# Kernel optimization log

Hardware: AMD Instinct MI355X
Metric: run time of the kernel (lower is better)

## Reference

```python
import jax, jax.numpy as jnp
import numpy as np


def _global_softmax(h):
    # Faithful to soft(): exp over ALL elements, divide by total sum (flattened).
    m = jnp.max(h)  # global max for numerical stability
    e = jnp.exp(h - m)
    return e / jnp.sum(e)


def setup_inputs() -> dict:
    key = jax.random.key(0)
    ks = jax.random.split(key, 7)
    B = 262144
    return {
        "x": jax.random.normal(ks[0], (B, 256), dtype=jnp.float32),
        "wz1": jax.random.normal(ks[1], (256, 64), dtype=jnp.float32) * 0.05,
        "b1": jax.random.normal(ks[2], (1, 64), dtype=jnp.float32),
        "wz2": jax.random.normal(ks[3], (64, 16), dtype=jnp.float32) * 0.1,
        "b2": jax.random.normal(ks[4], (1, 16), dtype=jnp.float32),
        "wz3": jax.random.normal(ks[5], (16, 4), dtype=jnp.float32) * 0.2,
        "b3": jax.random.normal(ks[6], (1, 4), dtype=jnp.float32),
    }


def reference(x, wz1, b1, wz2, b2, wz3, b3):
    h = jax.nn.relu(x @ wz1 + b1)          # [B,64]
    h = jnp.tanh(h @ wz2 + b2)             # [B,16]
    h = h @ wz3 + b3                       # [B,4]
    return _global_softmax(h)              # normalized over all B*4 elements
```

## Files before the change

### kernel.cpp

```cpp
#include <hip/hip_runtime.h>


typedef _Float16 half8 __attribute__((ext_vector_type(8)));
typedef _Float16 half4 __attribute__((ext_vector_type(4)));
typedef float f32x4 __attribute__((ext_vector_type(4)));

#define GRID 256
#define TPB  512
#define TROWS 64

#define XS  264
#define WS  264
#define H1S 72
#define W2S 72

#define SCALE_IN 256.0f
#define SCALE_W  2048.0f
#define INV_SC   (1.0f/524288.0f)

#define OFF_XH  0
#define OFF_XL  (OFF_XH + TROWS*XS*2)
#define OFF_W1H (OFF_XL + TROWS*XS*2)
#define OFF_W1L (OFF_W1H + 64*WS*2)
#define OFF_H1H (OFF_W1L + 64*WS*2)
#define OFF_H1L (OFF_H1H + TROWS*H1S*2)
#define OFF_W2H (OFF_H1L + TROWS*H1S*2)
#define OFF_W2L (OFF_W2H + 16*W2S*2)
#define OFF_SUM (OFF_W2L + 16*W2S*2)
#define SMEM_BYTES (OFF_SUM + 64*4)

extern __shared__ char smem_raw[];

#define MFMA16(a,b,c) __builtin_amdgcn_mfma_f32_16x16x32_f16((a),(b),(c),0,0,0)

__device__ __forceinline__ void lds_barrier() {
    asm volatile("s_waitcnt lgkmcnt(0)\ns_barrier" ::: "memory");
}

__global__ __launch_bounds__(TPB, 2) void fused_mlp(
    const float* __restrict__ x,
    const float* __restrict__ wz1, const float* __restrict__ b1,
    const float* __restrict__ wz2, const float* __restrict__ b2,
    const float* __restrict__ wz3, const float* __restrict__ b3,
    float* __restrict__ Eout, float* __restrict__ block_sums,
    int ntiles)
{
    _Float16* xh  = (_Float16*)(smem_raw + OFF_XH);
    _Float16* xl  = (_Float16*)(smem_raw + OFF_XL);
    _Float16* w1h = (_Float16*)(smem_raw + OFF_W1H);
    _Float16* w1l = (_Float16*)(smem_raw + OFF_W1L);
    _Float16* h1h = (_Float16*)(smem_raw + OFF_H1H);
    _Float16* h1l = (_Float16*)(smem_raw + OFF_H1L);
    _Float16* w2h = (_Float16*)(smem_raw + OFF_W2H);
    _Float16* w2l = (_Float16*)(smem_raw + OFF_W2L);
    float* sums   = (float*)(smem_raw + OFF_SUM);

    const int tid  = threadIdx.x;
    const int lane = tid & 63;
    const int wid  = __builtin_amdgcn_readfirstlane(tid >> 6);
    const int l15  = lane & 15;
    const int g8   = (lane >> 4) * 8;

    const size_t blk_row0 = (size_t)blockIdx.x * ntiles * TROWS;

    float4 xv[8];
    {
        const float4* xg = (const float4*)(x + blk_row0 * 256);
        #pragma unroll
        for (int c = 0; c < 8; ++c) xv[c] = xg[c * TPB + tid];
    }

    {
        const float4* wg = (const float4*)wz1;
        #pragma unroll
        for (int c = 0; c < 8; ++c) {
            const int q = c * TPB + tid;
            const float4 v = wg[q];
            const int k = q >> 4, n0 = (q & 15) * 4;
            const float vv[4] = {v.x, v.y, v.z, v.w};
            #pragma unroll
            for (int i = 0; i < 4; ++i) {
                const float s = vv[i] * SCALE_W;
                const _Float16 h = (_Float16)s;
                w1h[(n0 + i) * WS + k] = h;
                w1l[(n0 + i) * WS + k] = (_Float16)(s - (float)h);
            }
        }
        if (tid < 256) {
            const float4 v = ((const float4*)wz2)[tid];
            const int k = tid >> 2, c0 = (tid & 3) * 4;
            const float vv[4] = {v.x, v.y, v.z, v.w};
            #pragma unroll
            for (int i = 0; i < 4; ++i) {
                const float s = vv[i] * SCALE_W;
                const _Float16 h = (_Float16)s;
                w2h[(c0 + i) * W2S + k] = h;
                w2l[(c0 + i) * W2S + k] = (_Float16)(s - (float)h);
            }
        }
    }

    const int rt  = wid >> 1;
    const int ntp = wid & 1;
    const int col0 = (2 * ntp) * 16 + l15;
    const int col1 = (2 * ntp + 1) * 16 + l15;
    const float b1v0 = b1[col0], b1v1 = b1[col1];
    float b2v[4], w3v[4][4];
    #pragma unroll
    for (int i = 0; i < 4; ++i) {
        const int c2 = (lane >> 4) * 4 + i;
        b2v[i] = b2[c2];
        #pragma unroll
        for (int c3 = 0; c3 < 4; ++c3) w3v[i][c3] = wz3[c2 * 4 + c3];
    }
    const float b3v[4] = {b3[0], b3[1], b3[2], b3[3]};

    lds_barrier();

    half8 Bh[8][2];
    #pragma unroll
    for (int kt = 0; kt < 8; ++kt) {
        Bh[kt][0] = *(const half8*)(w1h + col0 * WS + kt * 32 + g8);
        Bh[kt][1] = *(const half8*)(w1h + col1 * WS + kt * 32 + g8);
    }
    half8 A2h[2], A2l[2];
    #pragma unroll
    for (int kt = 0; kt < 2; ++kt) {
        A2h[kt] = *(const half8*)(w2h + l15 * W2S + kt * 32 + g8);
        A2l[kt] = *(const half8*)(w2l + l15 * W2S + kt * 32 + g8);
    }

    float local_sum = 0.f;

    for (int t = 0; t < ntiles; ++t) {
        #pragma unroll
        for (int c = 0; c < 8; ++c) {
            const float vv[4] = {xv[c].x, xv[c].y, xv[c].z, xv[c].w};
            half4 hh, hl;
            #pragma unroll
            for (int i = 0; i < 4; ++i) {
                const float s = vv[i] * SCALE_IN;
                const _Float16 h = (_Float16)s;
                hh[i] = h;
                hl[i] = (_Float16)(s - (float)h);
            }
            const int row = c * 8 + wid;
            *(half4*)(xh + row * XS + lane * 4) = hh;
            *(half4*)(xl + row * XS + lane * 4) = hl;
        }
        if (t + 1 < ntiles) {
            const float4* xg2 =
                (const float4*)(x + (blk_row0 + (size_t)(t + 1) * TROWS) * 256);
            #pragma unroll
            for (int c = 0; c < 8; ++c) xv[c] = xg2[c * TPB + tid];
        }
        lds_barrier();

        f32x4 acc0 = {0.f, 0.f, 0.f, 0.f}, acc1 = {0.f, 0.f, 0.f, 0.f};
        {
            const _Float16* xh_p = xh + (rt * 16 + l15) * XS;
            const _Float16* xl_p = xl + (rt * 16 + l15) * XS;
            const _Float16* wl_p0 = w1l + col0 * WS;
            const _Float16* wl_p1 = w1l + col1 * WS;
            #pragma unroll
            for (int kt = 0; kt < 8; ++kt) {
                const int ko = kt * 32 + g8;
                const half8 ah  = *(const half8*)(xh_p + ko);
                const half8 al  = *(const half8*)(xl_p + ko);
                const half8 bl0 = *(const half8*)(wl_p0 + ko);
                const half8 bl1 = *(const half8*)(wl_p1 + ko);
                acc0 = MFMA16(ah, Bh[kt][0], acc0);
                acc1 = MFMA16(ah, Bh[kt][1], acc1);
                acc0 = MFMA16(al, Bh[kt][0], acc0);
                acc1 = MFMA16(al, Bh[kt][1], acc1);
                acc0 = MFMA16(ah, bl0, acc0);
                acc1 = MFMA16(ah, bl1, acc1);
            }
        }
        #pragma unroll
        for (int i = 0; i < 4; ++i) {
            const int r = rt * 16 + (lane >> 4) * 4 + i;
            const float h0 = fmaxf(fmaf(acc0[i], INV_SC, b1v0), 0.f);
            const float h1f = fmaxf(fmaf(acc1[i], INV_SC, b1v1), 0.f);
            const float s0 = h0 * SCALE_IN;
            const _Float16 h0h = (_Float16)s0;
            h1h[r * H1S + col0] = h0h;
            h1l[r * H1S + col0] = (_Float16)(s0 - (float)h0h);
            const float s1 = h1f * SCALE_IN;
            const _Float16 h1hh = (_Float16)s1;
            h1h[r * H1S + col1] = h1hh;
            h1l[r * H1S + col1] = (_Float16)(s1 - (float)h1hh);
        }
        lds_barrier();

        if (wid < 4) {
            f32x4 a2 = {0.f, 0.f, 0.f, 0.f};
            const _Float16* hh_p = h1h + (wid * 16 + l15) * H1S;
            const _Float16* hl_p = h1l + (wid * 16 + l15) * H1S;
            #pragma unroll
            for (int kt = 0; kt < 2; ++kt) {
                const int ko = kt * 32 + g8;
                const half8 bh = *(const half8*)(hh_p + ko);
                const half8 bl = *(const half8*)(hl_p + ko);
                a2 = MFMA16(A2h[kt], bh, a2);
                a2 = MFMA16(A2l[kt], bh, a2);
                a2 = MFMA16(A2h[kt], bl, a2);
            }
            float p0 = 0.f, p1 = 0.f, p2 = 0.f, p3 = 0.f;
            #pragma unroll
            for (int i = 0; i < 4; ++i) {
                const float h2 = tanhf(fmaf(a2[i], INV_SC, b2v[i]));
                p0 = fmaf(h2, w3v[i][0], p0);
                p1 = fmaf(h2, w3v[i][1], p1);
                p2 = fmaf(h2, w3v[i][2], p2);
                p3 = fmaf(h2, w3v[i][3], p3);
            }
            p0 += __shfl_xor(p0, 16, 64); p0 += __shfl_xor(p0, 32, 64);
            p1 += __shfl_xor(p1, 16, 64); p1 += __shfl_xor(p1, 32, 64);
            p2 += __shfl_xor(p2, 16, 64); p2 += __shfl_xor(p2, 32, 64);
            p3 += __shfl_xor(p3, 16, 64); p3 += __shfl_xor(p3, 32, 64);
            if (lane < 16) {
                const float e0 = expf(p0 + b3v[0]);
                const float e1 = expf(p1 + b3v[1]);
                const float e2 = expf(p2 + b3v[2]);
                const float e3 = expf(p3 + b3v[3]);
                const size_t row = blk_row0 + (size_t)t * TROWS + wid * 16 + lane;
                float4 ev; ev.x = e0; ev.y = e1; ev.z = e2; ev.w = e3;
                *(float4*)(Eout + row * 4) = ev;
                local_sum += (e0 + e1) + (e2 + e3);
            }
        }
    }

    #pragma unroll
    for (int off = 32; off > 0; off >>= 1)
        local_sum += __shfl_down(local_sum, off, 64);
    if (lane == 0) sums[wid] = local_sum;
    lds_barrier();
    if (tid == 0) {
        float s = 0.f;
        #pragma unroll
        for (int w = 0; w < 8; ++w) s += sums[w];
        block_sums[blockIdx.x] = s;
    }
}

__global__ __launch_bounds__(256) void reduce_kernel(
    const float* __restrict__ block_sums, float* __restrict__ s_inv)
{
    __shared__ float red[256];
    float s = 0.f;
    for (int i = threadIdx.x; i < GRID; i += 256) s += block_sums[i];
    red[threadIdx.x] = s;
    __syncthreads();
    #pragma unroll
    for (int o = 128; o > 0; o >>= 1) {
        if (threadIdx.x < o) red[threadIdx.x] += red[threadIdx.x + o];
        __syncthreads();
    }
    if (threadIdx.x == 0) s_inv[0] = 1.0f / red[0];
}

__global__ __launch_bounds__(256) void scale_kernel(
    float* __restrict__ out, const float* __restrict__ s_inv)
{
    const float inv = s_inv[0];
    const int idx = blockIdx.x * 256 + threadIdx.x;
    float4* o4 = (float4*)out;
    float4 v = o4[idx];
    v.x *= inv; v.y *= inv; v.z *= inv; v.w *= inv;
    o4[idx] = v;
}

extern "C" void kernel_launch(void* const* d_in, const int* in_sizes, int n_in,
                              void* d_out, int out_size, void* d_ws, size_t ws_size,
                              hipStream_t stream) {
    (void)n_in; (void)ws_size;
    const float* x   = (const float*)d_in[0];
    const float* wz1 = (const float*)d_in[1];
    const float* b1  = (const float*)d_in[2];
    const float* wz2 = (const float*)d_in[3];
    const float* b2  = (const float*)d_in[4];
    const float* wz3 = (const float*)d_in[5];
    const float* b3  = (const float*)d_in[6];
    float* out = (float*)d_out;

    float* wsf = (float*)d_ws;
    float* s_inv = wsf;
    float* block_sums = wsf + 1;

    const int B = in_sizes[0] / 256;
    const int ntiles = B / (GRID * TROWS);

    hipFuncSetAttribute((const void*)fused_mlp,
                        hipFuncAttributeMaxDynamicSharedMemorySize, SMEM_BYTES);

    fused_mlp<<<GRID, TPB, SMEM_BYTES, stream>>>(
        x, wz1, b1, wz2, b2, wz3, b3, out, block_sums, ntiles);
    reduce_kernel<<<1, 256, 0, stream>>>(block_sums, s_inv);

    const int n4 = out_size / 4;
    scale_kernel<<<n4 / 256, 256, 0, stream>>>(out, s_inv);
}
```

Before: 62.60 us.

## Stream x tiles into LDS via async global_load_lds with double buffering

Replaces the register prefetch and fp16 hi/lo LDS stores of x with direct global-to-LDS async loads into two XOR-swizzled fp32 buffers. The hi/lo split now happens after the LDS read, just before the MFMAs. W1 hi and lo fragments are held entirely in registers, and h1 is stored as fp32 in LDS. The separate reduce kernel is folded into the scale kernel, which removes one launch. LDS use roughly doubles and register pressure rises from the extra Bl fragments, which may limit occupancy at two blocks per CU.

```diff
diff --git a/kernel.cpp b/kernel.cpp
--- a/kernel.cpp
+++ b/kernel.cpp
@@ -2,39 +2,52 @@
 
 
 typedef _Float16 half8 __attribute__((ext_vector_type(8)));
-typedef _Float16 half4 __attribute__((ext_vector_type(4)));
 typedef float f32x4 __attribute__((ext_vector_type(4)));
 
 #define GRID 256
 #define TPB  512
 #define TROWS 64
 
-#define XS  264
-#define WS  264
-#define H1S 72
-#define W2S 72
-
 #define SCALE_IN 256.0f
 #define SCALE_W  2048.0f
 #define INV_SC   (1.0f/524288.0f)
 
-#define OFF_XH  0
-#define OFF_XL  (OFF_XH + TROWS*XS*2)
-#define OFF_W1H (OFF_XL + TROWS*XS*2)
-#define OFF_W1L (OFF_W1H + 64*WS*2)
-#define OFF_H1H (OFF_W1L + 64*WS*2)
-#define OFF_H1L (OFF_H1H + TROWS*H1S*2)
-#define OFF_W2H (OFF_H1L + TROWS*H1S*2)
-#define OFF_W2L (OFF_W2H + 16*W2S*2)
-#define OFF_SUM (OFF_W2L + 16*W2S*2)
-#define SMEM_BYTES (OFF_SUM + 64*4)
+#define XBUF_BYTES 65536
+#define OFF_H1 (2*XBUF_BYTES)
+#define H1S 68
+#define OFF_SUM (OFF_H1 + TROWS*H1S*4)
+#define SMEM_BYTES (OFF_SUM + 64)
 
 extern __shared__ char smem_raw[];
 
 #define MFMA16(a,b,c) __builtin_amdgcn_mfma_f32_16x16x32_f16((a),(b),(c),0,0,0)
 
-__device__ __forceinline__ void lds_barrier() {
-    asm volatile("s_waitcnt lgkmcnt(0)\ns_barrier" ::: "memory");
+__device__ __forceinline__ void gload16(const float* g, float* l) {
+    __builtin_amdgcn_global_load_lds(
+        (const __attribute__((address_space(1))) void*)g,
+        (__attribute__((address_space(3))) void*)l, 16, 0, 0);
+}
+
+__device__ __forceinline__ void stage_x(const float* xg_tile, char* xbuf,
+                                        int wid, int lane) {
+    #pragma unroll
+    for (int j = 0; j < 8; ++j) {
+        const int r = wid * 8 + j;
+        const float* src = xg_tile + (size_t)r * 256 + ((lane ^ j) << 2);
+        float* dst = (float*)(xbuf + r * 1024);
+        gload16(src, dst);
+    }
+}
+
+__device__ __forceinline__ void split8(const float* v, float scale,
+                                       half8& h, half8& l) {
+    #pragma unroll
+    for (int j = 0; j < 8; ++j) {
+        const float s = v[j] * scale;
+        const _Float16 hi = (_Float16)s;
+        h[j] = hi;
+        l[j] = (_Float16)(s - (float)hi);
+    }
 }
 
 __global__ __launch_bounds__(TPB, 2) void fused_mlp(
@@ -45,163 +58,125 @@
     float* __restrict__ Eout, float* __restrict__ block_sums,
     int ntiles)
 {
-    _Float16* xh  = (_Float16*)(smem_raw + OFF_XH);
-    _Float16* xl  = (_Float16*)(smem_raw + OFF_XL);
-    _Float16* w1h = (_Float16*)(smem_raw + OFF_W1H);
-    _Float16* w1l = (_Float16*)(smem_raw + OFF_W1L);
-    _Float16* h1h = (_Float16*)(smem_raw + OFF_H1H);
-    _Float16* h1l = (_Float16*)(smem_raw + OFF_H1L);
-    _Float16* w2h = (_Float16*)(smem_raw + OFF_W2H);
-    _Float16* w2l = (_Float16*)(smem_raw + OFF_W2L);
-    float* sums   = (float*)(smem_raw + OFF_SUM);
+    float* h1p  = (float*)(smem_raw + OFF_H1);
+    float* sums = (float*)(smem_raw + OFF_SUM);
 
     const int tid  = threadIdx.x;
     const int lane = tid & 63;
     const int wid  = __builtin_amdgcn_readfirstlane(tid >> 6);
     const int l15  = lane & 15;
-    const int g8   = (lane >> 4) * 8;
+    const int g4   = lane >> 4;
+    const int g8   = g4 * 8;
 
     const size_t blk_row0 = (size_t)blockIdx.x * ntiles * TROWS;
 
-    float4 xv[8];
+    stage_x(x + blk_row0 * 256, smem_raw, wid, lane);
     {
-        const float4* xg = (const float4*)(x + blk_row0 * 256);
-        #pragma unroll
-        for (int c = 0; c < 8; ++c) xv[c] = xg[c * TPB + tid];
-    }
-
-    {
-        const float4* wg = (const float4*)wz1;
-        #pragma unroll
-        for (int c = 0; c < 8; ++c) {
-            const int q = c * TPB + tid;
-            const float4 v = wg[q];
-            const int k = q >> 4, n0 = (q & 15) * 4;
-            const float vv[4] = {v.x, v.y, v.z, v.w};
-            #pragma unroll
-            for (int i = 0; i < 4; ++i) {
-                const float s = vv[i] * SCALE_W;
-                const _Float16 h = (_Float16)s;
-                w1h[(n0 + i) * WS + k] = h;
-                w1l[(n0 + i) * WS + k] = (_Float16)(s - (float)h);
-            }
-        }
-        if (tid < 256) {
-            const float4 v = ((const float4*)wz2)[tid];
-            const int k = tid >> 2, c0 = (tid & 3) * 4;
-            const float vv[4] = {v.x, v.y, v.z, v.w};
-            #pragma unroll
-            for (int i = 0; i < 4; ++i) {
-                const float s = vv[i] * SCALE_W;
-                const _Float16 h = (_Float16)s;
-                w2h[(c0 + i) * W2S + k] = h;
-                w2l[(c0 + i) * W2S + k] = (_Float16)(s - (float)h);
-            }
-        }
-    }
-
-    const int rt  = wid >> 1;
-    const int ntp = wid & 1;
-    const int col0 = (2 * ntp) * 16 + l15;
-    const int col1 = (2 * ntp + 1) * 16 + l15;
+        float* w1s = (float*)(smem_raw + XBUF_BYTES);
+        #pragma unroll
+        for (int j = 0; j < 8; ++j)
+            gload16(wz1 + wid * 2048 + j * 256 + lane * 4,
+                    w1s + wid * 2048 + j * 256);
+    }
+
+    const int rt   = wid >> 1;
+    const int ntp  = wid & 1;
+    const int col0 = ntp * 32 + l15;
+    const int col1 = col0 + 16;
     const float b1v0 = b1[col0], b1v1 = b1[col1];
     float b2v[4], w3v[4][4];
     #pragma unroll
     for (int i = 0; i < 4; ++i) {
-        const int c2 = (lane >> 4) * 4 + i;
+        const int c2 = g4 * 4 + i;
         b2v[i] = b2[c2];
         #pragma unroll
         for (int c3 = 0; c3 < 4; ++c3) w3v[i][c3] = wz3[c2 * 4 + c3];
     }
     const float b3v[4] = {b3[0], b3[1], b3[2], b3[3]};
 
-    lds_barrier();
-
-    half8 Bh[8][2];
-    #pragma unroll
-    for (int kt = 0; kt < 8; ++kt) {
-        Bh[kt][0] = *(const half8*)(w1h + col0 * WS + kt * 32 + g8);
-        Bh[kt][1] = *(const half8*)(w1h + col1 * WS + kt * 32 + g8);
-    }
     half8 A2h[2], A2l[2];
     #pragma unroll
     for (int kt = 0; kt < 2; ++kt) {
-        A2h[kt] = *(const half8*)(w2h + l15 * W2S + kt * 32 + g8);
-        A2l[kt] = *(const half8*)(w2l + l15 * W2S + kt * 32 + g8);
-    }
-
+        float tmp[8];
+        #pragma unroll
+        for (int j = 0; j < 8; ++j) tmp[j] = wz2[(kt * 32 + g8 + j) * 16 + l15];
+        split8(tmp, SCALE_W, A2h[kt], A2l[kt]);
+    }
+
+    asm volatile("s_waitcnt vmcnt(0)\ns_barrier" ::: "memory");
+
+    half8 Bh[8][2], Bl[8][2];
+    {
+        const float* w1s = (const float*)(smem_raw + XBUF_BYTES);
+        #pragma unroll
+        for (int kt = 0; kt < 8; ++kt) {
+            float t0[8], t1[8];
+            #pragma unroll
+            for (int j = 0; j < 8; ++j) {
+                const int k = kt * 32 + g8 + j;
+                t0[j] = w1s[k * 64 + col0];
+                t1[j] = w1s[k * 64 + col1];
+            }
+            split8(t0, SCALE_W, Bh[kt][0], Bl[kt][0]);
+            split8(t1, SCALE_W, Bh[kt][1], Bl[kt][1]);
+        }
+    }
+    asm volatile("s_waitcnt lgkmcnt(0)\ns_barrier" ::: "memory");
+
+    const int arow = rt * 16 + l15;
+    const int sw   = l15 & 7;
     float local_sum = 0.f;
 
     for (int t = 0; t < ntiles; ++t) {
-        #pragma unroll
-        for (int c = 0; c < 8; ++c) {
-            const float vv[4] = {xv[c].x, xv[c].y, xv[c].z, xv[c].w};
-            half4 hh, hl;
-            #pragma unroll
-            for (int i = 0; i < 4; ++i) {
-                const float s = vv[i] * SCALE_IN;
-                const _Float16 h = (_Float16)s;
-                hh[i] = h;
-                hl[i] = (_Float16)(s - (float)h);
-            }
-            const int row = c * 8 + wid;
-            *(half4*)(xh + row * XS + lane * 4) = hh;
-            *(half4*)(xl + row * XS + lane * 4) = hl;
-        }
+        const char* xb = smem_raw + (t & 1) * XBUF_BYTES;
         if (t + 1 < ntiles) {
-            const float4* xg2 =
-                (const float4*)(x + (blk_row0 + (size_t)(t + 1) * TROWS) * 256);
-            #pragma unroll
-            for (int c = 0; c < 8; ++c) xv[c] = xg2[c * TPB + tid];
-        }
-        lds_barrier();
+            stage_x(x + (blk_row0 + (size_t)(t + 1) * TROWS) * 256,
+                    smem_raw + ((t + 1) & 1) * XBUF_BYTES, wid, lane);
+            asm volatile("s_waitcnt vmcnt(8)\ns_barrier" ::: "memory");
+        } else {
+            asm volatile("s_waitcnt vmcnt(0)\ns_barrier" ::: "memory");
+        }
 
         f32x4 acc0 = {0.f, 0.f, 0.f, 0.f}, acc1 = {0.f, 0.f, 0.f, 0.f};
         {
-            const _Float16* xh_p = xh + (rt * 16 + l15) * XS;
-            const _Float16* xl_p = xl + (rt * 16 + l15) * XS;
-            const _Float16* wl_p0 = w1l + col0 * WS;
-            const _Float16* wl_p1 = w1l + col1 * WS;
+            const char* xrow = xb + arow * 1024;
             #pragma unroll
             for (int kt = 0; kt < 8; ++kt) {
-                const int ko = kt * 32 + g8;
-                const half8 ah  = *(const half8*)(xh_p + ko);
-                const half8 al  = *(const half8*)(xl_p + ko);
-                const half8 bl0 = *(const half8*)(wl_p0 + ko);
-                const half8 bl1 = *(const half8*)(wl_p1 + ko);
+                const int c0 = kt * 8 + 2 * g4;
+                const float4 lo = *(const float4*)(xrow + ((c0 ^ sw) << 4));
+                const float4 hi = *(const float4*)(xrow + (((c0 + 1) ^ sw) << 4));
+                const float v[8] = {lo.x, lo.y, lo.z, lo.w,
+                                    hi.x, hi.y, hi.z, hi.w};
+                half8 ah, al;
+                split8(v, SCALE_IN, ah, al);
                 acc0 = MFMA16(ah, Bh[kt][0], acc0);
                 acc1 = MFMA16(ah, Bh[kt][1], acc1);
                 acc0 = MFMA16(al, Bh[kt][0], acc0);
                 acc1 = MFMA16(al, Bh[kt][1], acc1);
-                acc0 = MFMA16(ah, bl0, acc0);
-                acc1 = MFMA16(ah, bl1, acc1);
+                acc0 = MFMA16(ah, Bl[kt][0], acc0);
+                acc1 = MFMA16(ah, Bl[kt][1], acc1);
             }
         }
         #pragma unroll
         for (int i = 0; i < 4; ++i) {
-            const int r = rt * 16 + (lane >> 4) * 4 + i;
-            const float h0 = fmaxf(fmaf(acc0[i], INV_SC, b1v0), 0.f);
-            const float h1f = fmaxf(fmaf(acc1[i], INV_SC, b1v1), 0.f);
-            const float s0 = h0 * SCALE_IN;
-            const _Float16 h0h = (_Float16)s0;
-            h1h[r * H1S + col0] = h0h;
-            h1l[r * H1S + col0] = (_Float16)(s0 - (float)h0h);
-            const float s1 = h1f * SCALE_IN;
-            const _Float16 h1hh = (_Float16)s1;
-            h1h[r * H1S + col1] = h1hh;
-            h1l[r * H1S + col1] = (_Float16)(s1 - (float)h1hh);
-        }
-        lds_barrier();
+            const int r = rt * 16 + g4 * 4 + i;
+            h1p[r * H1S + col0] = fmaxf(fmaf(acc0[i], INV_SC, b1v0), 0.f);
+            h1p[r * H1S + col1] = fmaxf(fmaf(acc1[i], INV_SC, b1v1), 0.f);
+        }
+        asm volatile("s_waitcnt lgkmcnt(0)\ns_barrier" ::: "memory");
 
         if (wid < 4) {
+            const float* hrow = h1p + (wid * 16 + l15) * H1S;
             f32x4 a2 = {0.f, 0.f, 0.f, 0.f};
-            const _Float16* hh_p = h1h + (wid * 16 + l15) * H1S;
-            const _Float16* hl_p = h1l + (wid * 16 + l15) * H1S;
             #pragma unroll
             for (int kt = 0; kt < 2; ++kt) {
-                const int ko = kt * 32 + g8;
-                const half8 bh = *(const half8*)(hh_p + ko);
-                const half8 bl = *(const half8*)(hl_p + ko);
+                const int k0 = kt * 32 + g8;
+                const float4 lo = *(const float4*)(hrow + k0);
+                const float4 hi = *(const float4*)(hrow + k0 + 4);
+                const float v[8] = {lo.x, lo.y, lo.z, lo.w,
+                                    hi.x, hi.y, hi.z, hi.w};
+                half8 bh, bl;
+                split8(v, SCALE_IN, bh, bl);
                 a2 = MFMA16(A2h[kt], bh, a2);
                 a2 = MFMA16(A2l[kt], bh, a2);
                 a2 = MFMA16(A2h[kt], bl, a2);
@@ -236,7 +211,7 @@
     for (int off = 32; off > 0; off >>= 1)
         local_sum += __shfl_down(local_sum, off, 64);
     if (lane == 0) sums[wid] = local_sum;
-    lds_barrier();
+    asm volatile("s_waitcnt lgkmcnt(0)\ns_barrier" ::: "memory");
     if (tid == 0) {
         float s = 0.f;
         #pragma unroll
@@ -245,27 +220,18 @@
     }
 }
 
-__global__ __launch_bounds__(256) void reduce_kernel(
-    const float* __restrict__ block_sums, float* __restrict__ s_inv)
+__global__ __launch_bounds__(256) void scale_kernel(
+    float* __restrict__ out, const float* __restrict__ block_sums)
 {
-    __shared__ float red[256];
-    float s = 0.f;
-    for (int i = threadIdx.x; i < GRID; i += 256) s += block_sums[i];
-    red[threadIdx.x] = s;
+    __shared__ float red[4];
+    const int tid = threadIdx.x;
+    float s = block_sums[tid];
+    #pragma unroll
+    for (int off = 32; off > 0; off >>= 1) s += __shfl_down(s, off, 64);
+    if ((tid & 63) == 0) red[tid >> 6] = s;
     __syncthreads();
-    #pragma unroll
-    for (int o = 128; o > 0; o >>= 1) {
-        if (threadIdx.x < o) red[threadIdx.x] += red[threadIdx.x + o];
-        __syncthreads();
-    }
-    if (threadIdx.x == 0) s_inv[0] = 1.0f / red[0];
-}
-
-__global__ __launch_bounds__(256) void scale_kernel(
-    float* __restrict__ out, const float* __restrict__ s_inv)
-{
-    const float inv = s_inv[0];
-    const int idx = blockIdx.x * 256 + threadIdx.x;
+    const float inv = 1.0f / ((red[0] + red[1]) + (red[2] + red[3]));
+    const int idx = blockIdx.x * 256 + tid;
     float4* o4 = (float4*)out;
     float4 v = o4[idx];
     v.x *= inv; v.y *= inv; v.z *= inv; v.w *= inv;
@@ -285,9 +251,7 @@
     const float* b3  = (const float*)d_in[6];
     float* out = (float*)d_out;
 
-    float* wsf = (float*)d_ws;
-    float* s_inv = wsf;
-    float* block_sums = wsf + 1;
+    float* block_sums = (float*)d_ws;
 
     const int B = in_sizes[0] / 256;
     const int ntiles = B / (GRID * TROWS);
@@ -297,8 +261,7 @@
 
     fused_mlp<<<GRID, TPB, SMEM_BYTES, stream>>>(
         x, wz1, b1, wz2, b2, wz3, b3, out, block_sums, ntiles);
-    reduce_kernel<<<1, 256, 0, stream>>>(block_sums, s_inv);
 
     const int n4 = out_size / 4;
-    scale_kernel<<<n4 / 256, 256, 0, stream>>>(out, s_inv);
-}
+    scale_kernel<<<n4 / 256, 256, 0, stream>>>(out, block_sums);
+}
```

Measured after the change: 67.12 us. +7.2%, slower.

## Hoist low-half W1 fragments into registers and fold reduction into scale kernel

Applied to the files above, without the earlier changes.

Loads the low-precision part of the first-layer weights into registers once, before the tile loop, so the inner MFMA loop no longer rereads them from LDS each tile. It also removes the separate single-block reduce kernel. Each scale block now reduces the 256 block sums itself with wave shuffles and computes the inverse locally. This saves one kernel launch and a serial dependency, but adds 32 more half8 registers per thread (occupancy risk) and repeats the 256-element reduction in every scale block.

```diff
diff --git a/kernel.cpp b/kernel.cpp
--- a/kernel.cpp
+++ b/kernel.cpp
@@ -117,11 +117,13 @@
 
     lds_barrier();
 
-    half8 Bh[8][2];
+    half8 Bh[8][2], Bl[8][2];
     #pragma unroll
     for (int kt = 0; kt < 8; ++kt) {
         Bh[kt][0] = *(const half8*)(w1h + col0 * WS + kt * 32 + g8);
         Bh[kt][1] = *(const half8*)(w1h + col1 * WS + kt * 32 + g8);
+        Bl[kt][0] = *(const half8*)(w1l + col0 * WS + kt * 32 + g8);
+        Bl[kt][1] = *(const half8*)(w1l + col1 * WS + kt * 32 + g8);
     }
     half8 A2h[2], A2l[2];
     #pragma unroll
@@ -160,21 +162,17 @@
         {
             const _Float16* xh_p = xh + (rt * 16 + l15) * XS;
             const _Float16* xl_p = xl + (rt * 16 + l15) * XS;
-            const _Float16* wl_p0 = w1l + col0 * WS;
-            const _Float16* wl_p1 = w1l + col1 * WS;
             #pragma unroll
             for (int kt = 0; kt < 8; ++kt) {
                 const int ko = kt * 32 + g8;
-                const half8 ah  = *(const half8*)(xh_p + ko);
-                const half8 al  = *(const half8*)(xl_p + ko);
-                const half8 bl0 = *(const half8*)(wl_p0 + ko);
-                const half8 bl1 = *(const half8*)(wl_p1 + ko);
+                const half8 ah = *(const half8*)(xh_p + ko);
+                const half8 al = *(const half8*)(xl_p + ko);
                 acc0 = MFMA16(ah, Bh[kt][0], acc0);
                 acc1 = MFMA16(ah, Bh[kt][1], acc1);
                 acc0 = MFMA16(al, Bh[kt][0], acc0);
                 acc1 = MFMA16(al, Bh[kt][1], acc1);
-                acc0 = MFMA16(ah, bl0, acc0);
-                acc1 = MFMA16(ah, bl1, acc1);
+                acc0 = MFMA16(ah, Bl[kt][0], acc0);
+                acc1 = MFMA16(ah, Bl[kt][1], acc1);
             }
         }
         #pragma unroll
@@ -245,27 +243,18 @@
     }
 }
 
-__global__ __launch_bounds__(256) void reduce_kernel(
-    const float* __restrict__ block_sums, float* __restrict__ s_inv)
+__global__ __launch_bounds__(256) void scale_kernel(
+    float* __restrict__ out, const float* __restrict__ block_sums)
 {
-    __shared__ float red[256];
-    float s = 0.f;
-    for (int i = threadIdx.x; i < GRID; i += 256) s += block_sums[i];
-    red[threadIdx.x] = s;
+    __shared__ float red[4];
+    const int tid = threadIdx.x;
+    float s = block_sums[tid];
+    #pragma unroll
+    for (int off = 32; off > 0; off >>= 1) s += __shfl_down(s, off, 64);
+    if ((tid & 63) == 0) red[tid >> 6] = s;
     __syncthreads();
-    #pragma unroll
-    for (int o = 128; o > 0; o >>= 1) {
-        if (threadIdx.x < o) red[threadIdx.x] += red[threadIdx.x + o];
-        __syncthreads();
-    }
-    if (threadIdx.x == 0) s_inv[0] = 1.0f / red[0];
-}
-
-__global__ __launch_bounds__(256) void scale_kernel(
-    float* __restrict__ out, const float* __restrict__ s_inv)
-{
-    const float inv = s_inv[0];
-    const int idx = blockIdx.x * 256 + threadIdx.x;
+    const float inv = 1.0f / ((red[0] + red[1]) + (red[2] + red[3]));
+    const int idx = blockIdx.x * 256 + tid;
     float4* o4 = (float4*)out;
     float4 v = o4[idx];
     v.x *= inv; v.y *= inv; v.z *= inv; v.w *= inv;
@@ -285,9 +274,7 @@
     const float* b3  = (const float*)d_in[6];
     float* out = (float*)d_out;
 
-    float* wsf = (float*)d_ws;
-    float* s_inv = wsf;
-    float* block_sums = wsf + 1;
+    float* block_sums = (float*)d_ws;
 
     const int B = in_sizes[0] / 256;
     const int ntiles = B / (GRID * TROWS);
@@ -297,8 +284,7 @@
 
     fused_mlp<<<GRID, TPB, SMEM_BYTES, stream>>>(
         x, wz1, b1, wz2, b2, wz3, b3, out, block_sums, ntiles);
-    reduce_kernel<<<1, 256, 0, stream>>>(block_sums, s_inv);
 
     const int n4 = out_size / 4;
-    scale_kernel<<<n4 / 256, 256, 0, stream>>>(out, s_inv);
-}
+    scale_kernel<<<n4 / 256, 256, 0, stream>>>(out, block_sums);
+}
```

Result: faster. 57.34 us, median of 2 (-8.4%).

## Fuse reduce and scale into MLP kernel via cooperative grid sync; double-buffer x prefetch

Applied to the files above, without the earlier changes.

Replaces the separate reduce and scale kernels with a cooperative launch: after each block writes its partial sum, a grid-wide sync lets every block compute the global sum and rescale its own output rows in place. This removes two extra kernel launches and a separate pass over the output. The main loop is also unrolled by two with ping-pong register buffers so the next x tile load is issued before the current tile is converted. Risks are cooperative-launch overhead, the grid barrier cost, and higher register pressure from two x buffers. The loop also assumes an even tile count.

```diff
diff --git a/kernel.cpp b/kernel.cpp
--- a/kernel.cpp
+++ b/kernel.cpp
@@ -1,5 +1,8 @@
 #include <hip/hip_runtime.h>
-
+#include <hip/hip_cooperative_groups.h>
+
+
+namespace cg = cooperative_groups;
 
 typedef _Float16 half8 __attribute__((ext_vector_type(8)));
 typedef _Float16 half4 __attribute__((ext_vector_type(4)));
@@ -63,11 +66,11 @@
 
     const size_t blk_row0 = (size_t)blockIdx.x * ntiles * TROWS;
 
-    float4 xv[8];
+    float4 xva[8], xvb[8];
     {
         const float4* xg = (const float4*)(x + blk_row0 * 256);
         #pragma unroll
-        for (int c = 0; c < 8; ++c) xv[c] = xg[c * TPB + tid];
+        for (int c = 0; c < 8; ++c) xva[c] = xg[c * TPB + tid];
     }
 
     {
@@ -132,10 +135,16 @@
 
     float local_sum = 0.f;
 
-    for (int t = 0; t < ntiles; ++t) {
+    auto body = [&](float4 (&cur)[8], float4 (&nxt)[8], int t) {
+        if (t + 1 < ntiles) {
+            const float4* xg2 =
+                (const float4*)(x + (blk_row0 + (size_t)(t + 1) * TROWS) * 256);
+            #pragma unroll
+            for (int c = 0; c < 8; ++c) nxt[c] = xg2[c * TPB + tid];
+        }
         #pragma unroll
         for (int c = 0; c < 8; ++c) {
-            const float vv[4] = {xv[c].x, xv[c].y, xv[c].z, xv[c].w};
+            const float vv[4] = {cur[c].x, cur[c].y, cur[c].z, cur[c].w};
             half4 hh, hl;
             #pragma unroll
             for (int i = 0; i < 4; ++i) {
@@ -147,12 +156,6 @@
             const int row = c * 8 + wid;
             *(half4*)(xh + row * XS + lane * 4) = hh;
             *(half4*)(xl + row * XS + lane * 4) = hl;
-        }
-        if (t + 1 < ntiles) {
-            const float4* xg2 =
-                (const float4*)(x + (blk_row0 + (size_t)(t + 1) * TROWS) * 256);
-            #pragma unroll
-            for (int c = 0; c < 8; ++c) xv[c] = xg2[c * TPB + tid];
         }
         lds_barrier();
 
@@ -230,6 +233,11 @@
                 local_sum += (e0 + e1) + (e2 + e3);
             }
         }
+    };
+
+    for (int tp = 0; tp < ntiles; tp += 2) {
+        body(xva, xvb, tp);
+        body(xvb, xva, tp + 1);
     }
 
     #pragma unroll
@@ -243,39 +251,35 @@
         for (int w = 0; w < 8; ++w) s += sums[w];
         block_sums[blockIdx.x] = s;
     }
-}
-
-__global__ __launch_bounds__(256) void reduce_kernel(
-    const float* __restrict__ block_sums, float* __restrict__ s_inv)
-{
-    __shared__ float red[256];
-    float s = 0.f;
-    for (int i = threadIdx.x; i < GRID; i += 256) s += block_sums[i];
-    red[threadIdx.x] = s;
-    __syncthreads();
-    #pragma unroll
-    for (int o = 128; o > 0; o >>= 1) {
-        if (threadIdx.x < o) red[threadIdx.x] += red[threadIdx.x + o];
-        __syncthreads();
-    }
-    if (threadIdx.x == 0) s_inv[0] = 1.0f / red[0];
-}
-
-__global__ __launch_bounds__(256) void scale_kernel(
-    float* __restrict__ out, const float* __restrict__ s_inv)
-{
-    const float inv = s_inv[0];
-    const int idx = blockIdx.x * 256 + threadIdx.x;
-    float4* o4 = (float4*)out;
-    float4 v = o4[idx];
-    v.x *= inv; v.y *= inv; v.z *= inv; v.w *= inv;
-    o4[idx] = v;
+    __threadfence();
+
+    cg::this_grid().sync();
+
+    {
+        float s = 0.f;
+        if (wid < 4) s = block_sums[(wid << 6) | lane];
+        #pragma unroll
+        for (int off = 32; off > 0; off >>= 1) s += __shfl_down(s, off, 64);
+        if (wid < 4 && lane == 0) sums[wid] = s;
+        lds_barrier();
+        const float inv = 1.0f / ((sums[0] + sums[1]) + (sums[2] + sums[3]));
+
+        float4* o4 = (float4*)Eout;
+        const size_t base = blk_row0;
+        #pragma unroll
+        for (int i = 0; i < 2; ++i) {
+            const size_t idx = base + (size_t)i * TPB + tid;
+            float4 v = o4[idx];
+            v.x *= inv; v.y *= inv; v.z *= inv; v.w *= inv;
+            o4[idx] = v;
+        }
+    }
 }
 
 extern "C" void kernel_launch(void* const* d_in, const int* in_sizes, int n_in,
                               void* d_out, int out_size, void* d_ws, size_t ws_size,
                               hipStream_t stream) {
-    (void)n_in; (void)ws_size;
+    (void)n_in; (void)ws_size; (void)out_size;
     const float* x   = (const float*)d_in[0];
     const float* wz1 = (const float*)d_in[1];
     const float* b1  = (const float*)d_in[2];
@@ -285,20 +289,17 @@
     const float* b3  = (const float*)d_in[6];
     float* out = (float*)d_out;
 
-    float* wsf = (float*)d_ws;
-    float* s_inv = wsf;
-    float* block_sums = wsf + 1;
+    float* block_sums = (float*)d_ws;
 
     const int B = in_sizes[0] / 256;
-    const int ntiles = B / (GRID * TROWS);
+    int ntiles = B / (GRID * TROWS);
 
     hipFuncSetAttribute((const void*)fused_mlp,
                         hipFuncAttributeMaxDynamicSharedMemorySize, SMEM_BYTES);
 
-    fused_mlp<<<GRID, TPB, SMEM_BYTES, stream>>>(
-        x, wz1, b1, wz2, b2, wz3, b3, out, block_sums, ntiles);
-    reduce_kernel<<<1, 256, 0, stream>>>(block_sums, s_inv);
-
-    const int n4 = out_size / 4;
-    scale_kernel<<<n4 / 256, 256, 0, stream>>>(out, s_inv);
+    void* args[] = {(void*)&x, (void*)&wz1, (void*)&b1, (void*)&wz2,
+                    (void*)&b2, (void*)&wz3, (void*)&b3,
+                    (void*)&out, (void*)&block_sums, (void*)&ntiles};
+    hipLaunchCooperativeKernel((const void*)fused_mlp, dim3(GRID), dim3(TPB),
+                               args, SMEM_BYTES, stream);
 }
```

Measured after the change: 143.2 us. 2.29x slower.
